# Kernel tuning notes

Measured on AMD Instinct MI355X. Metric: run time of the kernel, lower is better.

The kernel has to match this reference:

```python
import jax, jax.numpy as jnp
import numpy as np

CHUNK = 64
MIN_CLAMP = 1e-6
EPS = 1e-5


def layer_norm(x, scale, bias):
    mu = jnp.mean(x, axis=-1, keepdims=True)
    var = jnp.var(x, axis=-1, keepdims=True)
    return (x - mu) / jnp.sqrt(var + EPS) * scale + bias


def group_norm(x, scale, bias, num_groups):
    # Faithful to the module's GroupNorm: stats over (all rows, within-group channels)
    shp = x.shape
    xr = x.reshape(-1, num_groups, shp[-1] // num_groups)
    mu = jnp.mean(xr, axis=(0, 2), keepdims=True)
    var = jnp.var(xr, axis=(0, 2), keepdims=True)
    xn = ((xr - mu) / jnp.sqrt(var + EPS)).reshape(shp)
    return xn * scale + bias


def time_shift(x):
    return jnp.pad(x[:, :-1], ((0, 0), (1, 0), (0, 0)))


def chunkwise_single(k, v, r, w, u, state):
    # one (batch*head) lane: k,v,r,w,u are (L, D); state is (D, D)
    C = CHUNK
    L, D = r.shape
    pad = (-L) % C
    if pad:
        padf = lambda a: jnp.pad(a, ((0, pad), (0, 0)))
        r, k, v, w, u = map(padf, (r, k, v, w, u))
    Lp = L + pad
    N = Lp // C
    r, k, v, w, u = (a.reshape(N, C, D) for a in (r, k, v, w, u))
    w = jnp.log(jnp.clip(w, MIN_CLAMP, 1.0))
    A = jnp.exp(jnp.cumsum(w, axis=1))                                    # (N,C,D)
    A_inter = jnp.exp(jax.lax.cumsum(w, axis=1, reverse=True) - w)        # (N,C,D)
    A_intra = jnp.cumsum(w, axis=1)                                       # (N,C,D)
    kv = jnp.einsum('ncj,nck->ncjk', A_inter * k, v)                      # (N,C,D,D)

    def scan_fn(s, inp):
        A_t, kv_t = inp
        return A_t * s + kv_t, s

    new_state, S = jax.lax.scan(scan_fn, state, (A.reshape(Lp, D), kv.reshape(Lp, D, D)))
    S = S.reshape(N, C, D, D)
    inter = jnp.einsum('ncj,ncjk->nck', r * jnp.exp(A_intra - w), S)

    mid = C // 2

    def intra_fn(rc, kc, vc, Ac, uc):
        r_decay = rc * jnp.exp(jnp.pad(Ac[:-1], ((1, 0), (0, 0))) - Ac[mid:mid + 1])
        k_decay = kc * jnp.exp(Ac[mid:mid + 1] - Ac)
        u_diag = jnp.diag(jnp.sum(rc * uc * kc, -1))
        return (jnp.tril(r_decay @ k_decay.T, -1) + u_diag) @ vc

    intra = jax.vmap(intra_fn)(r, k, v, A_intra, u)
    y = (inter + intra).reshape(Lp, D)[:L]
    return y, new_state


def _forward(x, state, time_maa_x, time_maa_w, time_maa_k, time_maa_v, time_maa_r, time_maa_g,
             time_decay, time_faaaa, time_maa_w1, time_maa_w2, time_decay_w1, time_decay_w2,
             Wr, Wk, Wv, Wg, Wo, ln_x_scale, ln_x_bias,
             time_maa_k_ch, time_maa_r_ch, Wk_ch, Wv_ch, Wr_ch,
             ln1_scale, ln1_bias, ln2_scale, ln2_bias):
    B, T, E = x.shape
    H, Sh = time_faaaa.shape
    # ---- time mixing (on ln1(x)) ----
    xn = layer_norm(x, ln1_scale, ln1_bias)
    sx = time_shift(xn) - xn
    xmix = xn + sx * time_maa_x
    t5 = jnp.tanh(xmix @ time_maa_w1).reshape(B, T, 5, -1).swapaxes(1, 2)    # (B,5,T,32)
    # faithful to original: batched matmul then reshape (B,5,T,E) -> (5,B,T,E)
    m = jnp.einsum('bgtc,gce->bgte', t5, time_maa_w2).reshape(5, B, T, E)
    mw, mk, mv, mr, mg = m
    xw = xn + sx * (time_maa_w + mw)
    xk = xn + sx * (time_maa_k + mk)
    xv = xn + sx * (time_maa_v + mv)
    xr = xn + sx * (time_maa_r + mr)
    xg = xn + sx * (time_maa_g + mg)
    r = (xr @ Wr).reshape(B, T, H, Sh)
    k = (xk @ Wk).reshape(B, T, H, Sh)
    v = (xv @ Wv).reshape(B, T, H, Sh)
    g = jax.nn.silu(xg @ Wg)                                                 # (B,T,H*Sh)
    off = (jnp.tanh(xw @ time_decay_w1) @ time_decay_w2).reshape(B, T, H, Sh)
    w = jax.nn.softplus(-(time_decay.reshape(1, 1, H, Sh) + off))
    u = jnp.broadcast_to(time_faaaa, (B, T, H, Sh))
    lane = lambda a: a.transpose(0, 2, 1, 3).reshape(B * H, T, Sh)
    y, new_state = jax.vmap(chunkwise_single)(lane(k), lane(v), lane(r), lane(w), lane(u),
                                              state.reshape(B * H, Sh, Sh))
    y = y.reshape(B, H, T, Sh).transpose(0, 2, 1, 3).reshape(B, T, H * Sh)
    y = group_norm(y, ln_x_scale, ln_x_bias, H)
    x = x + (y * g) @ Wo
    # ---- channel mixing (on ln2(x)) ----
    xn2 = layer_norm(x, ln2_scale, ln2_bias)
    sx2 = time_shift(xn2) - xn2
    kk = jax.nn.relu((xn2 + sx2 * time_maa_k_ch) @ Wk_ch) ** 2
    kv = kk @ Wv_ch
    out = x + jax.nn.sigmoid((xn2 + sx2 * time_maa_r_ch) @ Wr_ch) * kv
    return out, new_state.reshape(B, H, Sh, Sh)


def setup_inputs():
    B, T, E = 2, 512, 1024
    H, Sh, F = 16, 64, 4096
    D = H * Sh
    layer_id, n_layer = 12, 24
    r01 = layer_id / (n_layer - 1)
    r10 = 1.0 - layer_id / n_layer
    ar_e = np.arange(E, dtype=np.float64) / E
    maa = lambda p: jnp.asarray((1.0 - ar_e ** p).reshape(1, 1, E), jnp.float32)
    n = np.arange(D, dtype=np.float64)
    time_decay = jnp.asarray((-6 + 5 * (n / (D - 1)) ** (0.7 + 1.3 * r01)).reshape(1, D), jnp.float32)
    time_faaaa = jnp.asarray((r01 * (1 - n / (D - 1)) + ((n + 1) % 3 - 1) * 0.1).reshape(H, Sh), jnp.float32)
    key = jax.random.key(0)
    ks = jax.random.split(key, 14)
    uni = lambda kk, shp: jax.random.uniform(kk, shp, jnp.float32, 0.0, 1e-4)
    dense = lambda kk, i, o: jax.random.normal(kk, (i, o), jnp.float32) / np.float32(np.sqrt(i))
    return dict(
        x=jax.random.normal(ks[0], (B, T, E), jnp.float32),
        state=jnp.zeros((B, H, Sh, Sh), jnp.float32),
        time_maa_x=maa(r10), time_maa_w=maa(r10), time_maa_k=maa(r10),
        time_maa_v=maa(r10 + 0.3 * r01), time_maa_r=maa(0.5 * r10), time_maa_g=maa(0.5 * r10),
        time_decay=time_decay, time_faaaa=time_faaaa,
        time_maa_w1=uni(ks[1], (E, 5 * 32)), time_maa_w2=uni(ks[2], (5, 32, E)),
        time_decay_w1=uni(ks[3], (E, 64)), time_decay_w2=uni(ks[4], (64, E)),
        Wr=dense(ks[5], E, D), Wk=dense(ks[6], E, D), Wv=dense(ks[7], E, D),
        Wg=dense(ks[8], E, D), Wo=dense(ks[9], D, E),
        ln_x_scale=jnp.ones((D,), jnp.float32), ln_x_bias=jnp.zeros((D,), jnp.float32),
        time_maa_k_ch=maa(r10), time_maa_r_ch=maa(r10),
        Wk_ch=dense(ks[10], E, F), Wv_ch=dense(ks[11], F, E), Wr_ch=dense(ks[12], E, E),
        ln1_scale=jnp.ones((E,), jnp.float32), ln1_bias=jnp.zeros((E,), jnp.float32),
        ln2_scale=jnp.ones((E,), jnp.float32), ln2_bias=jnp.zeros((E,), jnp.float32),
    )


def reference(x, state, time_maa_x, time_maa_w, time_maa_k, time_maa_v, time_maa_r, time_maa_g,
              time_decay, time_faaaa, time_maa_w1, time_maa_w2, time_decay_w1, time_decay_w2,
              Wr, Wk, Wv, Wg, Wo, ln_x_scale, ln_x_bias,
              time_maa_k_ch, time_maa_r_ch, Wk_ch, Wv_ch, Wr_ch,
              ln1_scale, ln1_bias, ln2_scale, ln2_bias):
    return _forward(x, state, time_maa_x, time_maa_w, time_maa_k, time_maa_v, time_maa_r, time_maa_g,
                    time_decay, time_faaaa, time_maa_w1, time_maa_w2, time_decay_w1, time_decay_w2,
                    Wr, Wk, Wv, Wg, Wo, ln_x_scale, ln_x_bias,
                    time_maa_k_ch, time_maa_r_ch, Wk_ch, Wv_ch, Wr_ch,
                    ln1_scale, ln1_bias, ln2_scale, ln2_bias)
```

## Files before the change

### kernel.cpp

```cpp
#include <hip/hip_runtime.h>
#include <math.h>

#define T_  512
#define E_  1024
#define BTE 1048576

enum { EPI_NONE=0, EPI_TANH=1, EPI_SILU=2, EPI_RELU2=3, EPI_WLOG=4, EPI_ADDRES=5,
       EPI_SIGMUL4=6 };

typedef __attribute__((ext_vector_type(8))) short bf16x8;
typedef __attribute__((ext_vector_type(4))) float f32x4;

__device__ __forceinline__ unsigned short f2bf(float f) {
    union { float f; unsigned u; } v; v.f = f;
    unsigned r = v.u + 0x7fffu + ((v.u >> 16) & 1u);
    return (unsigned short)(r >> 16);
}
__device__ __forceinline__ float bf2f(unsigned short h) {
    union { unsigned u; float f; } v; v.u = ((unsigned)h) << 16;
    return v.f;
}

__global__ __launch_bounds__(256) void ln_rows_k(const float* __restrict__ x,
        const float* __restrict__ sc, const float* __restrict__ bi,
        float* __restrict__ out)
{
    const int row = blockIdx.x;
    const int tid = threadIdx.x;
    const float* xr = x + (size_t)row * E_;
    float4 v = *reinterpret_cast<const float4*>(xr + tid*4);
    float s  = v.x + v.y + v.z + v.w;
    float ss = v.x*v.x + v.y*v.y + v.z*v.z + v.w*v.w;
    #pragma unroll
    for (int off = 32; off > 0; off >>= 1) {
        s  += __shfl_down(s, off);
        ss += __shfl_down(ss, off);
    }
    __shared__ float ps[4], pss[4];
    __shared__ float smu, srstd;
    if ((tid & 63) == 0) { ps[tid>>6] = s; pss[tid>>6] = ss; }
    __syncthreads();
    if (tid == 0) {
        float S  = ps[0]+ps[1]+ps[2]+ps[3];
        float SS = pss[0]+pss[1]+pss[2]+pss[3];
        float mu  = S * (1.f/E_);
        float var = SS * (1.f/E_) - mu*mu;
        smu = mu; srstd = rsqrtf(var + 1e-5f);
    }
    __syncthreads();
    const float mu = smu, rstd = srstd;
    float4 s4 = *reinterpret_cast<const float4*>(sc + tid*4);
    float4 b4 = *reinterpret_cast<const float4*>(bi + tid*4);
    float4 o;
    o.x = (v.x-mu)*rstd*s4.x + b4.x;
    o.y = (v.y-mu)*rstd*s4.y + b4.y;
    o.z = (v.z-mu)*rstd*s4.z + b4.z;
    o.w = (v.w-mu)*rstd*s4.w + b4.w;
    *reinterpret_cast<float4*>(out + (size_t)row*E_ + tid*4) = o;
}

__global__ __launch_bounds__(256) void mix_x_k(const float* __restrict__ xn,
        const float* __restrict__ maa, unsigned short* __restrict__ out)
{
    int idx = blockIdx.x*256 + threadIdx.x;
    int e = idx & 1023;
    int t = (idx >> 10) & 511;
    float xv = xn[idx];
    float prev = t ? xn[idx - E_] : 0.f;
    out[idx] = f2bf(xv + (prev - xv) * maa[e]);
}

__global__ __launch_bounds__(256) void mix_ch_k(const float* __restrict__ xn2,
        const float* __restrict__ maaK, const float* __restrict__ maaR,
        unsigned short* __restrict__ ak, unsigned short* __restrict__ ar)
{
    int idx = blockIdx.x*256 + threadIdx.x;
    int e = idx & 1023;
    int t = (idx >> 10) & 511;
    float xv = xn2[idx];
    float prev = t ? xn2[idx - E_] : 0.f;
    float sxv = prev - xv;
    ak[idx] = f2bf(xv + sxv * maaK[e]);
    ar[idx] = f2bf(xv + sxv * maaR[e]);
}

__global__ __launch_bounds__(256) void t5red_k(const float* __restrict__ tp,
        unsigned short* __restrict__ t5p)
{
    int idx = blockIdx.x*256 + threadIdx.x;
    int c = idx & 63, bt = (idx >> 6) & 1023, g = idx >> 16;
    unsigned short o = 0;
    if (c < 32) {
        float s = 0.f;
        size_t off = (size_t)bt*160 + g*32 + c;
        #pragma unroll
        for (int z = 0; z < 8; ++z) s += tp[(size_t)z*163840 + off];
        o = f2bf(tanhf(s));
    }
    t5p[idx] = o;
}

__global__ __launch_bounds__(256) void dw1red_k(const float* __restrict__ dp,
        unsigned short* __restrict__ h)
{
    int idx = blockIdx.x*256 + threadIdx.x;
    float s = 0.f;
    #pragma unroll
    for (int z = 0; z < 8; ++z) s += dp[(size_t)z*65536 + idx];
    h[idx] = f2bf(tanhf(s));
}

__global__ __launch_bounds__(256) void mix5_apply_k(const float* __restrict__ xn,
        const unsigned short* __restrict__ mb,
        const float* __restrict__ maaW, const float* __restrict__ maaK,
        const float* __restrict__ maaV, const float* __restrict__ maaR,
        const float* __restrict__ maaG,
        unsigned short* __restrict__ xw, unsigned short* __restrict__ xk,
        unsigned short* __restrict__ xv, unsigned short* __restrict__ xr,
        unsigned short* __restrict__ xg)
{
    int idx = blockIdx.x*256 + threadIdx.x;
    int e = idx & 1023;
    int bt = idx >> 10;
    int b = bt >> 9, t = bt & 511;
    float xnv = xn[idx];
    float prev = t ? xn[idx - E_] : 0.f;
    float sxv = prev - xnv;
    float m[5];
    #pragma unroll
    for (int o = 0; o < 5; ++o) {
        int L = o*2 + b;
        int bs = L / 5, gs = L - bs*5;
        m[o] = bf2f(mb[(size_t)gs*1048576 + (size_t)(bs*T_ + t)*E_ + e]);
    }
    xw[idx] = f2bf(xnv + sxv*(maaW[e] + m[0]));
    xk[idx] = f2bf(xnv + sxv*(maaK[e] + m[1]));
    xv[idx] = f2bf(xnv + sxv*(maaV[e] + m[2]));
    xr[idx] = f2bf(xnv + sxv*(maaR[e] + m[3]));
    xg[idx] = f2bf(xnv + sxv*(maaG[e] + m[4]));
}

struct WTA {
    const float* src[16];
    unsigned short* dst[16];
    int K[16], N[16], Npad[16], Kpad[16], tx[16];
    int cum[17];
};
__global__ __launch_bounds__(256) void wtransall_k(WTA a)
{
    int bid = blockIdx.x;
    int s = 0;
    while (bid >= a.cum[s+1]) ++s;
    const int local = bid - a.cum[s];
    const int bx = local % a.tx[s];
    const int by = local / a.tx[s];
    const float* S = a.src[s];
    unsigned short* D = a.dst[s];
    const int K = a.K[s], N = a.N[s], Npad = a.Npad[s], Kpad = a.Kpad[s];
    __shared__ float t[64][65];
    const int tid = threadIdx.x;
    const int k0 = by*64, n0 = bx*64;
    #pragma unroll
    for (int i = 0; i < 16; ++i) {
        int r = i*4 + (tid >> 6), c = tid & 63;
        int gk = k0 + r, gn = n0 + c;
        t[r][c] = (gk < K && gn < N) ? S[(size_t)gk*N + gn] : 0.f;
    }
    __syncthreads();
    #pragma unroll
    for (int i = 0; i < 16; ++i) {
        int r = i*4 + (tid >> 6), c = tid & 63;
        int gn = n0 + r, gk = k0 + c;
        if (gn < Npad && gk < Kpad)
            D[(size_t)gn*Kpad + gk] = f2bf(t[c][r]);
    }
}

struct GemmArgs {
    const unsigned short* A[8];
    const unsigned short* B[8];
    void* C[8];
    const float* p1[8];
    const float* p2[8];
    int epi[8];
    int obf[8];
    int k0[8];
    int M, N, K, ldK;
};
__global__ __launch_bounds__(256) void mgemm_k(GemmArgs g)
{
    const int bz = blockIdx.z;
    const unsigned short* Ag = g.A[bz];
    const unsigned short* BT = g.B[bz];
    const int N = g.N, K = g.K;
    const int gx = gridDim.x, gy = gridDim.y;
    const int lin = blockIdx.x + gx*blockIdx.y;
    const int q = (gx*gy) >> 3;
    const int tile = (lin & 7)*q + (lin >> 3);
    const int bx = tile / gy;
    const int by = tile - bx*gy;
    const int m0 = by * 64, n0 = bx * 64;
    const int tid = threadIdx.x;
    const int lane = tid & 63, w = tid >> 6;

    __shared__ __align__(16) unsigned short As[2][4096];
    __shared__ __align__(16) unsigned short Bs[2][4096];

    const size_t rowBytes = (size_t)g.ldK * 2;
    int sI[4], sIsB[4]; size_t sOff[4];
    #pragma unroll
    for (int ii = 0; ii < 4; ++ii) {
        int t = w*4 + ii;
        int isB = t >> 3;
        int i = t & 7;
        int r = i*8 + (lane >> 3);
        int gb = ((lane & 7) * 16) ^ ((r & 7) << 4);
        sI[ii] = i; sIsB[ii] = isB;
        int srow = (isB ? n0 : m0) + r;
        sOff[ii] = (size_t)srow * rowBytes + gb;
    }
    auto stage = [&](int buf, size_t kbyte) {
        #pragma unroll
        for (int ii = 0; ii < 4; ++ii) {
            const char* src = (const char*)(sIsB[ii] ? BT : Ag) + sOff[ii] + kbyte;
            unsigned short* dst = (sIsB[ii] ? Bs[buf] : As[buf]) + sI[ii]*512;
            auto g1 = (const __attribute__((address_space(1))) unsigned int*)(src);
            auto l3 = (__attribute__((address_space(3))) unsigned int*)(uintptr_t)(dst);
            __builtin_amdgcn_global_load_lds(g1, l3, 16, 0, 0);
        }
    };

    const int wm = (w >> 1) * 32, wn = (w & 1) * 32;
    const int lr = lane & 15, lk = lane >> 4;
    int aoff[2][2], boff[2][2];
    #pragma unroll
    for (int mi = 0; mi < 2; ++mi)
        #pragma unroll
        for (int kw = 0; kw < 2; ++kw) {
            int ar = wm + mi*16 + lr;
            aoff[mi][kw] = ar*128 + ((kw*64 + lk*16) ^ ((ar & 7) << 4));
            int br = wn + mi*16 + lr;
            boff[mi][kw] = br*128 + ((kw*64 + lk*16) ^ ((br & 7) << 4));
        }

    f32x4 acc[2][2] = {};
    const size_t kbase = (size_t)g.k0[bz] * 2;
    stage(0, kbase);
    const int nk = K >> 6;
    int cur = 0;
    for (int kt = 0; kt < nk; ++kt) {
        __syncthreads();
        if (kt + 1 < nk) stage(cur ^ 1, kbase + (size_t)(kt + 1) * 128);
        const char* Ab = (const char*)As[cur];
        const char* Bb = (const char*)Bs[cur];
        bf16x8 af[2][2], bfv[2][2];
        #pragma unroll
        for (int mi = 0; mi < 2; ++mi)
            #pragma unroll
            for (int kw = 0; kw < 2; ++kw) {
                af[mi][kw]  = *(const bf16x8*)(Ab + aoff[mi][kw]);
                bfv[mi][kw] = *(const bf16x8*)(Bb + boff[mi][kw]);
            }
        #pragma unroll
        for (int kw = 0; kw < 2; ++kw)
            #pragma unroll
            for (int mi = 0; mi < 2; ++mi)
                #pragma unroll
                for (int ni = 0; ni < 2; ++ni)
                    acc[mi][ni] = __builtin_amdgcn_mfma_f32_16x16x32_bf16(
                        af[mi][kw], bfv[ni][kw], acc[mi][ni], 0, 0, 0);
        cur ^= 1;
    }

    const int epi = g.epi[bz], obf = g.obf[bz];
    const float* p1 = g.p1[bz];
    const float* p2 = g.p2[bz];
    float* Cf = (float*)g.C[bz];
    unsigned short* Ch = (unsigned short*)g.C[bz];
    #pragma unroll
    for (int mi = 0; mi < 2; ++mi) {
        #pragma unroll
        for (int ni = 0; ni < 2; ++ni) {
            #pragma unroll
            for (int j = 0; j < 4; ++j) {
                int gm = m0 + wm + mi*16 + lk*4 + j;
                int gn = n0 + wn + ni*16 + lr;
                if (gn >= N) continue;
                size_t idx = (size_t)gm * N + gn;
                float a = acc[mi][ni][j];
                float o = a;
                if (epi == EPI_TANH)        o = tanhf(a);
                else if (epi == EPI_SILU)   o = a / (1.f + expf(-a));
                else if (epi == EPI_RELU2)  { float r = fmaxf(a, 0.f); o = r*r; }
                else if (epi == EPI_WLOG) {
                    float z = -(p1[gn] + a);
                    float sp = (z > 15.f) ? z : log1pf(expf(z));
                    o = logf(fminf(fmaxf(sp, 1e-6f), 1.f));
                }
                else if (epi == EPI_ADDRES) o = a + p1[idx];
                else if (epi == EPI_SIGMUL4) {
                    float kvs = p1[idx] + p1[idx + BTE] + p1[idx + 2*BTE] + p1[idx + 3*BTE];
                    o = p2[idx] + kvs / (1.f + expf(-a));
                }
                if (obf) Ch[idx] = f2bf(o); else Cf[idx] = o;
            }
        }
    }
}

#define SWZI(r, c)  (((r) << 6) + ((c) ^ (((r) & 7) << 3)))
#define FIDX(r, kw) (((r) << 6) + ((((kw)*32) + fk*8) ^ (((r) & 7) << 3)))
__global__ __launch_bounds__(512) void chunk1_k(
    const unsigned short* __restrict__ rb, const unsigned short* __restrict__ kb,
    const unsigned short* __restrict__ vb,
    const unsigned short* __restrict__ hdecb, const unsigned short* __restrict__ dw2T,
    const float* __restrict__ tdecay, const float* __restrict__ faaaa,
    float* __restrict__ ypart, float* __restrict__ Ug,
    unsigned short* __restrict__ RDimg, unsigned short* __restrict__ BFb,
    float* __restrict__ B63g)
{
    const int blk = blockIdx.x;
    const int bh = blk >> 3, nc = blk & 7;
    const int b = bh >> 4, h = bh & 15;
    const int tid = threadIdx.x;
    const int l = tid & 63, w = tid >> 6;
    const int jl = l, q = w;
    const int fr = l & 15, fk = l >> 4;
    const int wm = (w >> 2) * 32, wn = (w & 3) * 16;
    const int t0 = nc * 64;

    __shared__ float sBF[64*66];
    __shared__ float sQS[8][64];
    __shared__ float sUD[64];
    __shared__ __align__(16) unsigned short sRDb [4096];
    __shared__ __align__(16) unsigned short sKAb [4096];
    __shared__ __align__(16) unsigned short sKA2b[4096];
    __shared__ __align__(16) unsigned short sKATb[4096];
    __shared__ __align__(16) unsigned short sVTb [4096];
    __shared__ __align__(16) unsigned short sVXTb[4096];
    __shared__ __align__(16) unsigned short sQMb [4096];
    __shared__ __align__(16) unsigned short sPMb [4096];

    const float u_reg = faaaa[h*64 + jl];
    const size_t base = (size_t)b*T_*E_ + (size_t)h*64;
    const size_t coff = (size_t)blk * 4096;

    {
        const int isB = w >> 2;
        #pragma unroll
        for (int ii = 0; ii < 2; ++ii) {
            const int i = (w & 3)*2 + ii;
            const int r = i*8 + (l >> 3);
            const int gb = ((l & 7)*16) ^ ((r & 7) << 4);
            const char* src = isB
                ? ((const char*)dw2T  + (size_t)(h*64 + r)*128 + gb)
                : ((const char*)hdecb + (size_t)(b*T_ + t0 + r)*128 + gb);
            unsigned short* dst = (isB ? sPMb : sQMb) + i*512;
            auto g1 = (const __attribute__((address_space(1))) unsigned int*)(src);
            auto l3 = (__attribute__((address_space(3))) unsigned int*)(uintptr_t)(dst);
            __builtin_amdgcn_global_load_lds(g1, l3, 16, 0, 0);
        }
    }
    __syncthreads();

    {
        f32x4 accO[2] = {};
        #pragma unroll
        for (int kw = 0; kw < 2; ++kw) {
            bf16x8 aH0 = *(const bf16x8*)(&sQMb[FIDX(wm + fr, kw)]);
            bf16x8 aH1 = *(const bf16x8*)(&sQMb[FIDX(wm + 16 + fr, kw)]);
            bf16x8 bD  = *(const bf16x8*)(&sPMb[FIDX(wn + fr, kw)]);
            accO[0] = __builtin_amdgcn_mfma_f32_16x16x32_bf16(aH0, bD, accO[0], 0,0,0);
            accO[1] = __builtin_amdgcn_mfma_f32_16x16x32_bf16(aH1, bD, accO[1], 0,0,0);
        }
        const float td = tdecay[h*64 + wn + fr];
        #pragma unroll
        for (int mi = 0; mi < 2; ++mi)
            #pragma unroll
            for (int reg = 0; reg < 4; ++reg) {
                const int t = wm + mi*16 + fk*4 + reg;
                const int col = wn + fr;
                float z = -(td + accO[mi][reg]);
                float sp = (z > 15.f) ? z : log1pf(expf(z));
                sBF[t*66 + col] = logf(fminf(fmaxf(sp, 1e-6f), 1.f));
            }
    }
    __syncthreads();

    float loc[8], vreg[8];
    {
        float cum = 0.f;
        #pragma unroll
        for (int c = 0; c < 8; ++c) {
            float wv = sBF[(q*8 + c)*66 + jl];
            cum += wv; loc[c] = cum;
        }
        sQS[q][jl] = cum;
    }
    __syncthreads();
    float pre = 0.f, atot = 0.f;
    #pragma unroll
    for (int qq = 0; qq < 8; ++qq) {
        float v = sQS[qq][jl];
        atot += v;
        if (qq < q) pre += v;
    }

    #pragma unroll
    for (int c = 0; c < 8; ++c) {
        const int t = q*8 + c;
        const size_t gi = base + (size_t)(t0 + t)*E_ + jl;
        const float rv = bf2f(rb[gi]), kv = bf2f(kb[gi]), vv = bf2f(vb[gi]);
        vreg[c] = vv;
        const float a = loc[c] + pre;
        const float aprev = (c > 0) ? (loc[c-1] + pre) : pre;
        sRDb [SWZI(t, jl)] = f2bf(rv * expf(aprev));
        const float ka = kv * expf(atot - a);
        sKAb [SWZI(t, jl)] = f2bf(ka);
        sKA2b[SWZI(t, jl)] = f2bf(kv * expf(-a));
        sKATb[SWZI(jl, t)] = f2bf(ka);
        sVTb [SWZI(jl, t)] = f2bf(vv);
        float p = rv * u_reg * kv;
        #pragma unroll
        for (int off = 32; off > 0; off >>= 1) p += __shfl_down(p, off);
        if (jl == 0) sUD[t] = p;
    }
    __syncthreads();

    f32x4 accQ[2] = {}, accP[2] = {};
    #pragma unroll
    for (int kw = 0; kw < 2; ++kw) {
        bf16x8 ar0 = *(const bf16x8*)(&sRDb[FIDX(wm + fr, kw)]);
        bf16x8 ar1 = *(const bf16x8*)(&sRDb[FIDX(wm + 16 + fr, kw)]);
        bf16x8 bka = *(const bf16x8*)(&sKAb [FIDX(wn + fr, kw)]);
        bf16x8 bk2 = *(const bf16x8*)(&sKA2b[FIDX(wn + fr, kw)]);
        accQ[0] = __builtin_amdgcn_mfma_f32_16x16x32_bf16(ar0, bk2, accQ[0], 0,0,0);
        accQ[1] = __builtin_amdgcn_mfma_f32_16x16x32_bf16(ar1, bk2, accQ[1], 0,0,0);
        accP[0] = __builtin_amdgcn_mfma_f32_16x16x32_bf16(ar0, bka, accP[0], 0,0,0);
        accP[1] = __builtin_amdgcn_mfma_f32_16x16x32_bf16(ar1, bka, accP[1], 0,0,0);
    }
    #pragma unroll
    for (int mi = 0; mi < 2; ++mi)
        #pragma unroll
        for (int reg = 0; reg < 4; ++reg) {
            int t = wm + mi*16 + fk*4 + reg;
            int s = wn + fr;
            float qv = (s < t) ? accQ[mi][reg] : ((s == t) ? sUD[t] : 0.f);
            float pv = (s < t) ? accP[mi][reg] : 0.f;
            sQMb[SWZI(t, s)] = f2bf(qv);
            sPMb[SWZI(t, s)] = f2bf(pv);
        }

    float loc2[8];
    {
        float cum2 = 0.f;
        #pragma unroll
        for (int c = 0; c < 8; ++c) {
            cum2 += loc[c] + pre;
            loc2[c] = cum2;
        }
        sQS[q][jl] = cum2;
    }
    __syncthreads();
    {
        float pre2 = 0.f;
        #pragma unroll
        for (int qq = 0; qq < 8; ++qq) if (qq < q) pre2 += sQS[qq][jl];
        #pragma unroll
        for (int c = 0; c < 8; ++c) {
            const int t = q*8 + c;
            const float Bv = loc2[c] + pre2;
            const float Bprev = (c > 0) ? (loc2[c-1] + pre2) : pre2;
            const float bfv = expf(Bprev);
            sBF[t*66 + jl] = bfv;
            BFb[coff + t*64 + jl] = f2bf(bfv);
            sVXTb[SWZI(jl, t)] = f2bf(vreg[c] * expf(-Bv));
            if (t == 63) B63g[(size_t)blk*64 + jl] = expf(Bv);
        }
    }
    __syncthreads();

    {
        f32x4 accI[2] = {}, accL[2] = {}, accU[2] = {};
        #pragma unroll
        for (int kw = 0; kw < 2; ++kw) {
            bf16x8 aQ0 = *(const bf16x8*)(&sQMb [FIDX(wm + fr, kw)]);
            bf16x8 aQ1 = *(const bf16x8*)(&sQMb [FIDX(wm + 16 + fr, kw)]);
            bf16x8 aP0 = *(const bf16x8*)(&sPMb [FIDX(wm + fr, kw)]);
            bf16x8 aP1 = *(const bf16x8*)(&sPMb [FIDX(wm + 16 + fr, kw)]);
            bf16x8 aK0 = *(const bf16x8*)(&sKATb[FIDX(wm + fr, kw)]);
            bf16x8 aK1 = *(const bf16x8*)(&sKATb[FIDX(wm + 16 + fr, kw)]);
            bf16x8 bV  = *(const bf16x8*)(&sVTb [FIDX(wn + fr, kw)]);
            bf16x8 bX  = *(const bf16x8*)(&sVXTb[FIDX(wn + fr, kw)]);
            accI[0] = __builtin_amdgcn_mfma_f32_16x16x32_bf16(aQ0, bV, accI[0], 0,0,0);
            accI[1] = __builtin_amdgcn_mfma_f32_16x16x32_bf16(aQ1, bV, accI[1], 0,0,0);
            accL[0] = __builtin_amdgcn_mfma_f32_16x16x32_bf16(aP0, bX, accL[0], 0,0,0);
            accL[1] = __builtin_amdgcn_mfma_f32_16x16x32_bf16(aP1, bX, accL[1], 0,0,0);
            accU[0] = __builtin_amdgcn_mfma_f32_16x16x32_bf16(aK0, bX, accU[0], 0,0,0);
            accU[1] = __builtin_amdgcn_mfma_f32_16x16x32_bf16(aK1, bX, accU[1], 0,0,0);
        }
        #pragma unroll
        for (int mi = 0; mi < 2; ++mi)
            #pragma unroll
            for (int reg = 0; reg < 4; ++reg) {
                int t = wm + mi*16 + fk*4 + reg;
                int k = wn + fr;
                float bfv = sBF[t*66 + k];
                ypart[base + (size_t)(t0 + t)*E_ + k] = accI[mi][reg] + bfv*accL[mi][reg];
                Ug[coff + t*64 + k] = accU[mi][reg];
            }
    }
    ((bf16x8*)(RDimg + coff))[tid] = ((const bf16x8*)sRDb)[tid];
}

__global__ __launch_bounds__(256) void chunk2_k(
    const float* __restrict__ st_in, const float* __restrict__ Ug,
    const float* __restrict__ B63g,
    unsigned short* __restrict__ Simg, float* __restrict__ st_out)
{
    const int bh = blockIdx.x;
    const int tid = threadIdx.x;
    __shared__ float S[4096];
    for (int i = tid; i < 4096; i += 256) S[i] = st_in[(size_t)bh*4096 + i];
    __syncthreads();
    const int k = tid >> 2, j0 = (tid & 3) * 16;
    for (int nc = 0; nc < 8; ++nc) {
        const size_t coff = ((size_t)bh*8 + nc) * 4096;
        #pragma unroll
        for (int hf = 0; hf < 2; ++hf) {
            bf16x8 tmp;
            #pragma unroll
            for (int e = 0; e < 8; ++e) tmp[e] = (short)f2bf(S[(j0 + hf*8 + e)*64 + k]);
            *(bf16x8*)(&Simg[coff + SWZI(k, j0 + hf*8)]) = tmp;
        }
        __syncthreads();
        for (int i = tid; i < 4096; i += 256) {
            int kk = i & 63;
            S[i] = B63g[((size_t)bh*8 + nc)*64 + kk] * (S[i] + Ug[coff + i]);
        }
        __syncthreads();
    }
    for (int i = tid; i < 4096; i += 256) st_out[(size_t)bh*4096 + i] = S[i];
}

__global__ __launch_bounds__(256) void chunk3_k(
    const unsigned short* __restrict__ RDimg, const unsigned short* __restrict__ Simg,
    const unsigned short* __restrict__ BFb, float* __restrict__ yb)
{
    const int blk = blockIdx.x;
    const int bh = blk >> 3, nc = blk & 7;
    const int b = bh >> 4, h = bh & 15;
    const int tid = threadIdx.x;
    const int l = tid & 63, w = tid >> 6;
    const int fr = l & 15, fk = l >> 4;
    const int wm = (w >> 1) * 32, wn = (w & 1) * 32;
    const int t0 = nc * 64;
    __shared__ __align__(16) unsigned short sRDb[4096];
    __shared__ __align__(16) unsigned short sSTb[4096];
    const size_t coff = (size_t)blk * 4096;

    #pragma unroll
    for (int ii = 0; ii < 2; ++ii) {
        int seg = (w*2 + ii) * 512;
        {
            auto g1 = (const __attribute__((address_space(1))) unsigned int*)(RDimg + coff + seg + (l << 3));
            auto l3 = (__attribute__((address_space(3))) unsigned int*)(uintptr_t)(sRDb + seg);
            __builtin_amdgcn_global_load_lds(g1, l3, 16, 0, 0);
        }
        {
            auto g1 = (const __attribute__((address_space(1))) unsigned int*)(Simg + coff + seg + (l << 3));
            auto l3 = (__attribute__((address_space(3))) unsigned int*)(uintptr_t)(sSTb + seg);
            __builtin_amdgcn_global_load_lds(g1, l3, 16, 0, 0);
        }
    }
    __syncthreads();

    f32x4 accS[2][2] = {};
    #pragma unroll
    for (int kw = 0; kw < 2; ++kw) {
        bf16x8 aR[2], bS[2];
        #pragma unroll
        for (int mi = 0; mi < 2; ++mi)
            aR[mi] = *(const bf16x8*)(&sRDb[FIDX(wm + mi*16 + fr, kw)]);
        #pragma unroll
        for (int ni = 0; ni < 2; ++ni)
            bS[ni] = *(const bf16x8*)(&sSTb[FIDX(wn + ni*16 + fr, kw)]);
        #pragma unroll
        for (int mi = 0; mi < 2; ++mi)
            #pragma unroll
            for (int ni = 0; ni < 2; ++ni)
                accS[mi][ni] = __builtin_amdgcn_mfma_f32_16x16x32_bf16(aR[mi], bS[ni], accS[mi][ni], 0,0,0);
    }
    const size_t base = (size_t)b*T_*E_ + (size_t)h*64;
    #pragma unroll
    for (int mi = 0; mi < 2; ++mi)
        #pragma unroll
        for (int ni = 0; ni < 2; ++ni)
            #pragma unroll
            for (int reg = 0; reg < 4; ++reg) {
                int t = wm + mi*16 + fk*4 + reg;
                int k = wn + ni*16 + fr;
                size_t gp = base + (size_t)(t0 + t)*E_ + k;
                yb[gp] += bf2f(BFb[coff + t*64 + k]) * accS[mi][ni][reg];
            }
}

__global__ __launch_bounds__(256) void gn_stats_k(const float* __restrict__ y,
        float* __restrict__ part)
{
    const int h = blockIdx.x, slab = blockIdx.y;
    const int tid = threadIdx.x;
    float s = 0.f, ss = 0.f;
    for (int i = tid; i < 2048; i += 256) {
        int r = slab*32 + (i >> 6), k = i & 63;
        float v = y[(size_t)r*E_ + h*64 + k];
        s += v; ss += v*v;
    }
    #pragma unroll
    for (int off = 32; off > 0; off >>= 1) {
        s  += __shfl_down(s, off);
        ss += __shfl_down(ss, off);
    }
    __shared__ float ps[4], pss[4];
    if ((tid & 63) == 0) { ps[tid>>6] = s; pss[tid>>6] = ss; }
    __syncthreads();
    if (tid == 0) {
        part[h*32 + slab]       = ps[0]+ps[1]+ps[2]+ps[3];
        part[512 + h*32 + slab] = pss[0]+pss[1]+pss[2]+pss[3];
    }
}

__global__ __launch_bounds__(256) void gn_apply_k(const float* __restrict__ y,
        const float* __restrict__ g, const float* __restrict__ part,
        const float* __restrict__ sc, const float* __restrict__ bi,
        unsigned short* __restrict__ z)
{
    __shared__ float smu[16], srs[16];
    const int tid = threadIdx.x;
    if (tid < 16) {
        float s = 0.f, ss = 0.f;
        #pragma unroll
        for (int sl = 0; sl < 32; ++sl) {
            s  += part[tid*32 + sl];
            ss += part[512 + tid*32 + sl];
        }
        float mu  = s * (1.f/65536.f);
        float var = ss * (1.f/65536.f) - mu*mu;
        smu[tid] = mu;
        srs[tid] = rsqrtf(var + 1e-5f);
    }
    __syncthreads();
    int idx = blockIdx.x*256 + tid;
    int d = idx & 1023;
    int h = d >> 6;
    float yn = (y[idx] - smu[h])*srs[h]*sc[d] + bi[d];
    z[idx] = f2bf(yn * g[idx]);
}

extern "C" void kernel_launch(void* const* d_in, const int* in_sizes, int n_in,
                              void* d_out, int out_size, void* d_ws, size_t ws_size,
                              hipStream_t stream)
{
    const float* x       = (const float*)d_in[0];
    const float* state0  = (const float*)d_in[1];
    const float* maa_x   = (const float*)d_in[2];
    const float* maa_w   = (const float*)d_in[3];
    const float* maa_k   = (const float*)d_in[4];
    const float* maa_v   = (const float*)d_in[5];
    const float* maa_r   = (const float*)d_in[6];
    const float* maa_g   = (const float*)d_in[7];
    const float* tdecay  = (const float*)d_in[8];
    const float* faaaa   = (const float*)d_in[9];
    const float* w1      = (const float*)d_in[10];
    const float* w2      = (const float*)d_in[11];
    const float* dw1     = (const float*)d_in[12];
    const float* dw2     = (const float*)d_in[13];
    const float* Wr      = (const float*)d_in[14];
    const float* Wk      = (const float*)d_in[15];
    const float* Wv      = (const float*)d_in[16];
    const float* Wg      = (const float*)d_in[17];
    const float* Wo      = (const float*)d_in[18];
    const float* lnx_s   = (const float*)d_in[19];
    const float* lnx_b   = (const float*)d_in[20];
    const float* maa_kch = (const float*)d_in[21];
    const float* maa_rch = (const float*)d_in[22];
    const float* Wk_ch   = (const float*)d_in[23];
    const float* Wv_ch   = (const float*)d_in[24];
    const float* Wr_ch   = (const float*)d_in[25];
    const float* ln1_s   = (const float*)d_in[26];
    const float* ln1_b   = (const float*)d_in[27];
    const float* ln2_s   = (const float*)d_in[28];
    const float* ln2_b   = (const float*)d_in[29];

    float* xn     = (float*)d_ws;
    float* t5dead = xn + 1048576;
    float* gbuf   = t5dead + 163840;
    float* wlogb  = gbuf + 1048576;
    float* ybuf   = wlogb + 1048576;
    float* kvb    = ybuf + 1048576;
    float* gnpart = kvb + 1048576;
    float* gnstat = gnpart + 1024;
    float* b63g   = gnstat + 32;
    unsigned short* u = (unsigned short*)(b63g + 16384);
    unsigned short* xmix = u;  u += 1048576;
    unsigned short* xw   = u;  u += 1048576;
    unsigned short* xk   = u;  u += 1048576;
    unsigned short* xv_  = u;  u += 1048576;
    unsigned short* xr   = u;  u += 1048576;
    unsigned short* xg   = u;  u += 1048576;
    unsigned short* xtr  = u;  u += 1048576;
    unsigned short* rb   = u;  u += 1048576;
    unsigned short* kb   = u;  u += 1048576;
    unsigned short* vb   = u;  u += 1048576;
    unsigned short* hdecb= u;  u += 65536;
    unsigned short* WrT  = u;  u += 1048576;
    unsigned short* WkT  = u;  u += 1048576;
    unsigned short* WvT  = u;  u += 1048576;
    unsigned short* WgT  = u;  u += 1048576;
    unsigned short* WoT  = u;  u += 1048576;
    unsigned short* WrchT= u;  u += 1048576;
    unsigned short* WkchT= u;  u += 4194304;
    unsigned short* WvchT= u;  u += 4194304;
    unsigned short* w1T  = u;  u += 196608;
    unsigned short* dw1T = u;  u += 65536;
    unsigned short* dw2T = u;  u += 65536;
    unsigned short* W2T5 = u;  u += 327680;
    unsigned short* t5p  = u;  u += 327680;
    unsigned short* zbuf  = xmix;
    unsigned short* akb   = xw;
    unsigned short* arb   = xk;
    unsigned short* kkb   = xv_;
    unsigned short* mb16  = (unsigned short*)wlogb;
    float*          Ug    = (float*)xv_;
    unsigned short* RDimg = xg;
    unsigned short* Simg  = xtr;
    unsigned short* BFb   = xmix;
    float* tpart = gbuf;
    float* dpart = (float*)xmix;
    float* kpart = gbuf;

    float* out   = (float*)d_out;
    float* x2buf = out;
    float* stout = out + (size_t)BTE;

    {
        WTA a{};
        const float* srcs[16] = {Wr, Wk, Wv, Wg, Wo, Wr_ch, Wk_ch, Wv_ch, w1, dw1, dw2,
                                 w2, w2+32768, w2+65536, w2+98304, w2+131072};
        unsigned short* dsts[16] = {WrT, WkT, WvT, WgT, WoT, WrchT, WkchT, WvchT,
                                    w1T, dw1T, dw2T,
                                    W2T5, W2T5+65536, W2T5+131072, W2T5+196608, W2T5+262144};
        int Ks[16]    = {1024,1024,1024,1024,1024,1024, 1024, 4096, 1024, 1024,   64, 32,32,32,32,32};
        int Ns[16]    = {1024,1024,1024,1024,1024,1024, 4096, 1024,  160,   64, 1024, 1024,1024,1024,1024,1024};
        int Npads[16] = {1024,1024,1024,1024,1024,1024, 4096, 1024,  192,   64, 1024, 1024,1024,1024,1024,1024};
        int Kpads[16] = {1024,1024,1024,1024,1024,1024, 1024, 4096, 1024, 1024,   64, 64,64,64,64,64};
        int cum = 0;
        for (int i = 0; i < 16; ++i) {
            a.src[i] = srcs[i]; a.dst[i] = dsts[i];
            a.K[i] = Ks[i]; a.N[i] = Ns[i]; a.Npad[i] = Npads[i]; a.Kpad[i] = Kpads[i];
            int txc = (Ns[i] + 63) / 64;
            int tyc = (Ks[i] + 63) / 64;
            a.tx[i] = txc;
            a.cum[i] = cum;
            cum += txc * tyc;
        }
        a.cum[16] = cum;
        wtransall_k<<<cum, 256, 0, stream>>>(a);
    }

    ln_rows_k<<<1024, 256, 0, stream>>>(x, ln1_s, ln1_b, xn);
    mix_x_k<<<4096, 256, 0, stream>>>(xn, maa_x, xmix);
    { GemmArgs g{}; g.M=1024; g.N=160; g.K=128; g.ldK=1024;
      for (int z = 0; z < 8; ++z) {
          g.A[z]=xmix; g.B[z]=w1T; g.C[z]=tpart + (size_t)z*163840;
          g.epi[z]=EPI_NONE; g.obf[z]=0; g.k0[z]=z*128;
      }
      mgemm_k<<<dim3(3,16,8), 256, 0, stream>>>(g); }
    t5red_k<<<1280, 256, 0, stream>>>(tpart, t5p);
    { GemmArgs g{}; g.M=1024; g.N=1024; g.K=64; g.ldK=64;
      for (int z = 0; z < 5; ++z) {
          g.A[z]=t5p + (size_t)z*65536; g.B[z]=W2T5 + (size_t)z*65536;
          g.C[z]=mb16 + (size_t)z*1048576; g.epi[z]=EPI_NONE; g.obf[z]=1;
      }
      mgemm_k<<<dim3(16,16,5), 256, 0, stream>>>(g); }
    mix5_apply_k<<<4096, 256, 0, stream>>>(xn, mb16, maa_w, maa_k, maa_v, maa_r, maa_g,
                                           xw, xk, xv_, xr, xg);
    { GemmArgs g{}; g.M=1024; g.N=1024; g.K=1024; g.ldK=1024;
      g.A[0]=xr;  g.B[0]=WrT; g.C[0]=rb;   g.epi[0]=EPI_NONE; g.obf[0]=1;
      g.A[1]=xk;  g.B[1]=WkT; g.C[1]=kb;   g.epi[1]=EPI_NONE; g.obf[1]=1;
      g.A[2]=xv_; g.B[2]=WvT; g.C[2]=vb;   g.epi[2]=EPI_NONE; g.obf[2]=1;
      g.A[3]=xg;  g.B[3]=WgT; g.C[3]=gbuf; g.epi[3]=EPI_SILU; g.obf[3]=0;
      mgemm_k<<<dim3(16,16,4), 256, 0, stream>>>(g); }
    { GemmArgs g{}; g.M=1024; g.N=64; g.K=128; g.ldK=1024;
      for (int z = 0; z < 8; ++z) {
          g.A[z]=xw; g.B[z]=dw1T; g.C[z]=dpart + (size_t)z*65536;
          g.epi[z]=EPI_NONE; g.obf[z]=0; g.k0[z]=z*128;
      }
      mgemm_k<<<dim3(1,16,8), 256, 0, stream>>>(g); }
    dw1red_k<<<256, 256, 0, stream>>>(dpart, hdecb);

    chunk1_k<<<256, 512, 0, stream>>>(rb, kb, vb, hdecb, dw2T, tdecay, faaaa,
                                      ybuf, Ug, RDimg, BFb, b63g);
    chunk2_k<<<32, 256, 0, stream>>>(state0, Ug, b63g, Simg, stout);
    chunk3_k<<<256, 256, 0, stream>>>(RDimg, Simg, BFb, ybuf);

    gn_stats_k<<<dim3(16,32), 256, 0, stream>>>(ybuf, gnpart);
    gn_apply_k<<<4096, 256, 0, stream>>>(ybuf, gbuf, gnpart, lnx_s, lnx_b, zbuf);
    { GemmArgs g{}; g.M=1024; g.N=1024; g.K=1024; g.ldK=1024;
      g.A[0]=zbuf; g.B[0]=WoT; g.C[0]=x2buf; g.epi[0]=EPI_ADDRES; g.obf[0]=0; g.p1[0]=x;
      mgemm_k<<<dim3(16,16,1), 256, 0, stream>>>(g); }

    ln_rows_k<<<1024, 256, 0, stream>>>(x2buf, ln2_s, ln2_b, xn);
    mix_ch_k<<<4096, 256, 0, stream>>>(xn, maa_kch, maa_rch, akb, arb);
    { GemmArgs g{}; g.M=1024; g.N=4096; g.K=1024; g.ldK=1024;
      g.A[0]=akb; g.B[0]=WkchT; g.C[0]=kkb; g.epi[0]=EPI_RELU2; g.obf[0]=1;
      mgemm_k<<<dim3(64,16,1), 256, 0, stream>>>(g); }
    { GemmArgs g{}; g.M=1024; g.N=1024; g.K=1024; g.ldK=4096;
      for (int z = 0; z < 4; ++z) {
          g.A[z]=kkb; g.B[z]=WvchT; g.C[z]=kpart + (size_t)z*BTE;
          g.epi[z]=EPI_NONE; g.obf[z]=0; g.k0[z]=z*1024;
      }
      mgemm_k<<<dim3(16,16,4), 256, 0, stream>>>(g); }
    { GemmArgs g{}; g.M=1024; g.N=1024; g.K=1024; g.ldK=1024;
      g.A[0]=arb; g.B[0]=WrchT; g.C[0]=out; g.epi[0]=EPI_SIGMUL4; g.obf[0]=0;
      g.p1[0]=kpart; g.p2[0]=x2buf;
      mgemm_k<<<dim3(16,16,1), 256, 0, stream>>>(g); }
}
```

Measured before the change: 211.2 us.

## Fuse layer norm with token-shift mix and shrink chunk1 shared memory

```diff
diff --git a/kernel.cpp b/kernel.cpp
--- a/kernel.cpp
+++ b/kernel.cpp
@@ -21,67 +21,118 @@
     return v.f;
 }
 
-__global__ __launch_bounds__(256) void ln_rows_k(const float* __restrict__ x,
+__global__ __launch_bounds__(256) void ln1mix_k(const float* __restrict__ x,
         const float* __restrict__ sc, const float* __restrict__ bi,
-        float* __restrict__ out)
+        const float* __restrict__ maa,
+        float* __restrict__ xn, unsigned short* __restrict__ xmix)
 {
     const int row = blockIdx.x;
+    const int t = row & 511;
     const int tid = threadIdx.x;
     const float* xr = x + (size_t)row * E_;
     float4 v = *reinterpret_cast<const float4*>(xr + tid*4);
-    float s  = v.x + v.y + v.z + v.w;
-    float ss = v.x*v.x + v.y*v.y + v.z*v.z + v.w*v.w;
+    float4 vp = make_float4(0.f, 0.f, 0.f, 0.f);
+    if (t) vp = *reinterpret_cast<const float4*>(xr - E_ + tid*4);
+    float s   = v.x + v.y + v.z + v.w;
+    float ss  = v.x*v.x + v.y*v.y + v.z*v.z + v.w*v.w;
+    float sp  = vp.x + vp.y + vp.z + vp.w;
+    float ssp = vp.x*vp.x + vp.y*vp.y + vp.z*vp.z + vp.w*vp.w;
     #pragma unroll
     for (int off = 32; off > 0; off >>= 1) {
-        s  += __shfl_down(s, off);
-        ss += __shfl_down(ss, off);
-    }
-    __shared__ float ps[4], pss[4];
-    __shared__ float smu, srstd;
-    if ((tid & 63) == 0) { ps[tid>>6] = s; pss[tid>>6] = ss; }
+        s   += __shfl_down(s, off);
+        ss  += __shfl_down(ss, off);
+        sp  += __shfl_down(sp, off);
+        ssp += __shfl_down(ssp, off);
+    }
+    __shared__ float p0[4], p1[4], p2[4], p3[4];
+    __shared__ float st[4];
+    if ((tid & 63) == 0) { p0[tid>>6]=s; p1[tid>>6]=ss; p2[tid>>6]=sp; p3[tid>>6]=ssp; }
     __syncthreads();
     if (tid == 0) {
-        float S  = ps[0]+ps[1]+ps[2]+ps[3];
-        float SS = pss[0]+pss[1]+pss[2]+pss[3];
+        float S  = p0[0]+p0[1]+p0[2]+p0[3];
+        float SS = p1[0]+p1[1]+p1[2]+p1[3];
+        float Sp = p2[0]+p2[1]+p2[2]+p2[3];
+        float SSp= p3[0]+p3[1]+p3[2]+p3[3];
         float mu  = S * (1.f/E_);
         float var = SS * (1.f/E_) - mu*mu;
-        smu = mu; srstd = rsqrtf(var + 1e-5f);
-    }
-    __syncthreads();
-    const float mu = smu, rstd = srstd;
+        float mup = Sp * (1.f/E_);
+        float varp= SSp * (1.f/E_) - mup*mup;
+        st[0] = mu; st[1] = rsqrtf(var + 1e-5f);
+        st[2] = mup; st[3] = rsqrtf(varp + 1e-5f);
+    }
+    __syncthreads();
+    const float mu = st[0], rstd = st[1], mup = st[2], rstdp = st[3];
     float4 s4 = *reinterpret_cast<const float4*>(sc + tid*4);
     float4 b4 = *reinterpret_cast<const float4*>(bi + tid*4);
-    float4 o;
-    o.x = (v.x-mu)*rstd*s4.x + b4.x;
-    o.y = (v.y-mu)*rstd*s4.y + b4.y;
-    o.z = (v.z-mu)*rstd*s4.z + b4.z;
-    o.w = (v.w-mu)*rstd*s4.w + b4.w;
-    *reinterpret_cast<float4*>(out + (size_t)row*E_ + tid*4) = o;
-}
-
-__global__ __launch_bounds__(256) void mix_x_k(const float* __restrict__ xn,
-        const float* __restrict__ maa, unsigned short* __restrict__ out)
-{
-    int idx = blockIdx.x*256 + threadIdx.x;
-    int e = idx & 1023;
-    int t = (idx >> 10) & 511;
-    float xv = xn[idx];
-    float prev = t ? xn[idx - E_] : 0.f;
-    out[idx] = f2bf(xv + (prev - xv) * maa[e]);
-}
-
-__global__ __launch_bounds__(256) void mix_ch_k(const float* __restrict__ xn2,
+    float xnv[4], prv[4];
+    xnv[0]=(v.x-mu)*rstd*s4.x+b4.x; xnv[1]=(v.y-mu)*rstd*s4.y+b4.y;
+    xnv[2]=(v.z-mu)*rstd*s4.z+b4.z; xnv[3]=(v.w-mu)*rstd*s4.w+b4.w;
+    prv[0]=t?(vp.x-mup)*rstdp*s4.x+b4.x:0.f; prv[1]=t?(vp.y-mup)*rstdp*s4.y+b4.y:0.f;
+    prv[2]=t?(vp.z-mup)*rstdp*s4.z+b4.z:0.f; prv[3]=t?(vp.w-mup)*rstdp*s4.w+b4.w:0.f;
+    float4 o; o.x=xnv[0]; o.y=xnv[1]; o.z=xnv[2]; o.w=xnv[3];
+    *reinterpret_cast<float4*>(xn + (size_t)row*E_ + tid*4) = o;
+    #pragma unroll
+    for (int j = 0; j < 4; ++j) {
+        int e = tid*4 + j;
+        xmix[(size_t)row*E_ + e] = f2bf(xnv[j] + (prv[j]-xnv[j])*maa[e]);
+    }
+}
+
+__global__ __launch_bounds__(256) void ln2mix_k(const float* __restrict__ x2,
+        const float* __restrict__ sc, const float* __restrict__ bi,
         const float* __restrict__ maaK, const float* __restrict__ maaR,
         unsigned short* __restrict__ ak, unsigned short* __restrict__ ar)
 {
-    int idx = blockIdx.x*256 + threadIdx.x;
-    int e = idx & 1023;
-    int t = (idx >> 10) & 511;
-    float xv = xn2[idx];
-    float prev = t ? xn2[idx - E_] : 0.f;
-    float sxv = prev - xv;
-    ak[idx] = f2bf(xv + sxv * maaK[e]);
-    ar[idx] = f2bf(xv + sxv * maaR[e]);
+    const int row = blockIdx.x;
+    const int t = row & 511;
+    const int tid = threadIdx.x;
+    const float* xr = x2 + (size_t)row * E_;
+    float4 v = *reinterpret_cast<const float4*>(xr + tid*4);
+    float4 vp = make_float4(0.f, 0.f, 0.f, 0.f);
+    if (t) vp = *reinterpret_cast<const float4*>(xr - E_ + tid*4);
+    float s   = v.x + v.y + v.z + v.w;
+    float ss  = v.x*v.x + v.y*v.y + v.z*v.z + v.w*v.w;
+    float sp  = vp.x + vp.y + vp.z + vp.w;
+    float ssp = vp.x*vp.x + vp.y*vp.y + vp.z*vp.z + vp.w*vp.w;
+    #pragma unroll
+    for (int off = 32; off > 0; off >>= 1) {
+        s   += __shfl_down(s, off);
+        ss  += __shfl_down(ss, off);
+        sp  += __shfl_down(sp, off);
+        ssp += __shfl_down(ssp, off);
+    }
+    __shared__ float p0[4], p1[4], p2[4], p3[4];
+    __shared__ float st[4];
+    if ((tid & 63) == 0) { p0[tid>>6]=s; p1[tid>>6]=ss; p2[tid>>6]=sp; p3[tid>>6]=ssp; }
+    __syncthreads();
+    if (tid == 0) {
+        float S  = p0[0]+p0[1]+p0[2]+p0[3];
+        float SS = p1[0]+p1[1]+p1[2]+p1[3];
+        float Sp = p2[0]+p2[1]+p2[2]+p2[3];
+        float SSp= p3[0]+p3[1]+p3[2]+p3[3];
+        float mu  = S * (1.f/E_);
+        float var = SS * (1.f/E_) - mu*mu;
+        float mup = Sp * (1.f/E_);
+        float varp= SSp * (1.f/E_) - mup*mup;
+        st[0] = mu; st[1] = rsqrtf(var + 1e-5f);
+        st[2] = mup; st[3] = rsqrtf(varp + 1e-5f);
+    }
+    __syncthreads();
+    const float mu = st[0], rstd = st[1], mup = st[2], rstdp = st[3];
+    float4 s4 = *reinterpret_cast<const float4*>(sc + tid*4);
+    float4 b4 = *reinterpret_cast<const float4*>(bi + tid*4);
+    float xnv[4], prv[4];
+    xnv[0]=(v.x-mu)*rstd*s4.x+b4.x; xnv[1]=(v.y-mu)*rstd*s4.y+b4.y;
+    xnv[2]=(v.z-mu)*rstd*s4.z+b4.z; xnv[3]=(v.w-mu)*rstd*s4.w+b4.w;
+    prv[0]=t?(vp.x-mup)*rstdp*s4.x+b4.x:0.f; prv[1]=t?(vp.y-mup)*rstdp*s4.y+b4.y:0.f;
+    prv[2]=t?(vp.z-mup)*rstdp*s4.z+b4.z:0.f; prv[3]=t?(vp.w-mup)*rstdp*s4.w+b4.w:0.f;
+    #pragma unroll
+    for (int j = 0; j < 4; ++j) {
+        int e = tid*4 + j;
+        float sxv = prv[j] - xnv[j];
+        ak[(size_t)row*E_ + e] = f2bf(xnv[j] + sxv*maaK[e]);
+        ar[(size_t)row*E_ + e] = f2bf(xnv[j] + sxv*maaR[e]);
+    }
 }
 
 __global__ __launch_bounds__(256) void t5red_k(const float* __restrict__ tp,
@@ -310,7 +361,7 @@
 
 #define SWZI(r, c)  (((r) << 6) + ((c) ^ (((r) & 7) << 3)))
 #define FIDX(r, kw) (((r) << 6) + ((((kw)*32) + fk*8) ^ (((r) & 7) << 3)))
-__global__ __launch_bounds__(512) void chunk1_k(
+__global__ __launch_bounds__(512, 4) void chunk1_k(
     const unsigned short* __restrict__ rb, const unsigned short* __restrict__ kb,
     const unsigned short* __restrict__ vb,
     const unsigned short* __restrict__ hdecb, const unsigned short* __restrict__ dw2T,
@@ -329,17 +380,18 @@
     const int wm = (w >> 2) * 32, wn = (w & 3) * 16;
     const int t0 = nc * 64;
 
-    __shared__ float sBF[64*66];
     __shared__ float sQS[8][64];
     __shared__ float sUD[64];
-    __shared__ __align__(16) unsigned short sRDb [4096];
-    __shared__ __align__(16) unsigned short sKAb [4096];
-    __shared__ __align__(16) unsigned short sKA2b[4096];
-    __shared__ __align__(16) unsigned short sKATb[4096];
-    __shared__ __align__(16) unsigned short sVTb [4096];
-    __shared__ __align__(16) unsigned short sVXTb[4096];
-    __shared__ __align__(16) unsigned short sQMb [4096];
-    __shared__ __align__(16) unsigned short sPMb [4096];
+    __shared__ __align__(16) unsigned short pool[32768];
+    unsigned short* sRDb  = pool;
+    unsigned short* sKAb  = pool + 4096;
+    unsigned short* sKA2b = pool + 8192;
+    unsigned short* sKATb = pool + 12288;
+    unsigned short* sVTb  = pool + 16384;
+    unsigned short* sVXTb = pool + 20480;
+    unsigned short* sQMb  = pool + 24576;
+    unsigned short* sPMb  = pool + 28672;
+    float* wlogf = (float*)(pool + 12288);
 
     const float u_reg = faaaa[h*64 + jl];
     const size_t base = (size_t)b*T_*E_ + (size_t)h*64;
@@ -382,7 +434,7 @@
                 const int col = wn + fr;
                 float z = -(td + accO[mi][reg]);
                 float sp = (z > 15.f) ? z : log1pf(expf(z));
-                sBF[t*66 + col] = logf(fminf(fmaxf(sp, 1e-6f), 1.f));
+                wlogf[t*64 + col] = logf(fminf(fmaxf(sp, 1e-6f), 1.f));
             }
     }
     __syncthreads();
@@ -392,7 +444,7 @@
         float cum = 0.f;
         #pragma unroll
         for (int c = 0; c < 8; ++c) {
-            float wv = sBF[(q*8 + c)*66 + jl];
+            float wv = wlogf[(q*8 + c)*64 + jl];
             cum += wv; loc[c] = cum;
         }
         sQS[q][jl] = cum;
@@ -471,9 +523,9 @@
             const int t = q*8 + c;
             const float Bv = loc2[c] + pre2;
             const float Bprev = (c > 0) ? (loc2[c-1] + pre2) : pre2;
-            const float bfv = expf(Bprev);
-            sBF[t*66 + jl] = bfv;
-            BFb[coff + t*64 + jl] = f2bf(bfv);
+            const unsigned short bfh = f2bf(expf(Bprev));
+            sKA2b[t*64 + jl] = bfh;
+            BFb[coff + t*64 + jl] = bfh;
             sVXTb[SWZI(jl, t)] = f2bf(vreg[c] * expf(-Bv));
             if (t == 63) B63g[(size_t)blk*64 + jl] = expf(Bv);
         }
@@ -505,7 +557,7 @@
             for (int reg = 0; reg < 4; ++reg) {
                 int t = wm + mi*16 + fk*4 + reg;
                 int k = wn + fr;
-                float bfv = sBF[t*66 + k];
+                float bfv = bf2f(sKA2b[t*64 + k]);
                 ypart[base + (size_t)(t0 + t)*E_ + k] = accI[mi][reg] + bfv*accL[mi][reg];
                 Ug[coff + t*64 + k] = accU[mi][reg];
             }
@@ -768,8 +820,7 @@
         wtransall_k<<<cum, 256, 0, stream>>>(a);
     }
 
-    ln_rows_k<<<1024, 256, 0, stream>>>(x, ln1_s, ln1_b, xn);
-    mix_x_k<<<4096, 256, 0, stream>>>(xn, maa_x, xmix);
+    ln1mix_k<<<1024, 256, 0, stream>>>(x, ln1_s, ln1_b, maa_x, xn, xmix);
     { GemmArgs g{}; g.M=1024; g.N=160; g.K=128; g.ldK=1024;
       for (int z = 0; z < 8; ++z) {
           g.A[z]=xmix; g.B[z]=w1T; g.C[z]=tpart + (size_t)z*163840;
@@ -810,8 +861,7 @@
       g.A[0]=zbuf; g.B[0]=WoT; g.C[0]=x2buf; g.epi[0]=EPI_ADDRES; g.obf[0]=0; g.p1[0]=x;
       mgemm_k<<<dim3(16,16,1), 256, 0, stream>>>(g); }
 
-    ln_rows_k<<<1024, 256, 0, stream>>>(x2buf, ln2_s, ln2_b, xn);
-    mix_ch_k<<<4096, 256, 0, stream>>>(xn, maa_kch, maa_rch, akb, arb);
+    ln2mix_k<<<1024, 256, 0, stream>>>(x2buf, ln2_s, ln2_b, maa_kch, maa_rch, akb, arb);
     { GemmArgs g{}; g.M=1024; g.N=4096; g.K=1024; g.ldK=1024;
       g.A[0]=akb; g.B[0]=WkchT; g.C[0]=kkb; g.epi[0]=EPI_RELU2; g.obf[0]=1;
       mgemm_k<<<dim3(64,16,1), 256, 0, stream>>>(g); }
```

Measured after the change: 209.0 us. About the same (-1.1%).
